# Performance work log

Hardware: AMD Instinct MI355X
Metric: run time of the kernel (lower is better)

## Reference

```python
import jax, jax.numpy as jnp
import numpy as np

B = 16      # number of point clouds
N = 16384   # points per cloud
K = 4096    # nb_vertices sampled per cloud (ratio = 0.25)


def _fps_single(pts, k):
    """Deterministic farthest-point sampling on one cloud.
    pts: [N, 3]. Start from index 0 (deterministic start), then iteratively
    pick the point with max min-distance to the selected set.
    Returns int32 indices [k].
    """
    mind0 = jnp.sum((pts - pts[0]) ** 2, axis=-1)  # [N] squared dists to seed

    def step(mind, _):
        idx = jnp.argmax(mind)                                   # farthest point
        d = jnp.sum((pts - pts[idx]) ** 2, axis=-1)              # [N]
        return jnp.minimum(mind, d), idx.astype(jnp.int32)

    _, idxs = jax.lax.scan(step, mind0, None, length=k - 1)
    return jnp.concatenate([jnp.zeros((1,), jnp.int32), idxs])


def setup_inputs() -> dict:
    key = jax.random.key(0)
    x = jax.random.normal(key, (B * N, 3), dtype=jnp.float32)
    batch = jnp.repeat(jnp.arange(B, dtype=jnp.int32), N)  # sorted cloud ids
    return {"x": x, "batch": batch}


def reference(x, batch):
    # ratio = K / N != 1, so the module runs fps and gathers.
    pts = x.reshape(B, N, 3)
    idxs = jax.vmap(lambda p: _fps_single(p, K))(pts)                 # [B, K]
    sampled = jnp.take_along_axis(pts, idxs[:, :, None], axis=1)      # [B, K, 3]
    x_out = sampled.reshape(B * K, 3)
    batch_out = jnp.repeat(jnp.arange(B, dtype=batch.dtype), K)       # [B*K]
    return (x_out, batch_out)
```

## Files before the change

kernel.cpp:

```cpp
#include <hip/hip_runtime.h>
#include <cstdint>

#pragma clang fp contract(off)

#define B_ 16
#define N_ 16384
#define K_ 4096
#define THREADS_ 1024
#define PTS_ (N_ / THREADS_)
#define NW_ (THREADS_ / 64)

#define PTS_LIST(X) \
  X(0) X(1) X(2) X(3) X(4) X(5) X(6) X(7) \
  X(8) X(9) X(10) X(11) X(12) X(13) X(14) X(15)

__device__ __forceinline__ float bfr(float f) {
  union { float f; uint32_t i; } c; c.f = f;
  c.i = (c.i + 0x7FFFu + ((c.i >> 16) & 1u)) & 0xFFFF0000u;
  return c.f;
}

template <int CTRL>
__device__ __forceinline__ unsigned long long kmax_dpp(unsigned long long k) {
  const int lo = (int)(unsigned)k;
  const int hi = (int)(unsigned)(k >> 32);
  const int plo = __builtin_amdgcn_update_dpp(lo, lo, CTRL, 0xF, 0xF, true);
  const int phi = __builtin_amdgcn_update_dpp(hi, hi, CTRL, 0xF, 0xF, true);
  const unsigned long long ok =
      ((unsigned long long)(unsigned)phi << 32) | (unsigned)plo;
  return ok > k ? ok : k;
}

__device__ __forceinline__ unsigned long long kmax_shfl(unsigned long long k, int m) {
  const int lo = __shfl_xor((int)(unsigned)k, m, 64);
  const int hi = __shfl_xor((int)(unsigned)(k >> 32), m, 64);
  const unsigned long long ok =
      ((unsigned long long)(unsigned)hi << 32) | (unsigned)lo;
  return ok > k ? ok : k;
}

__device__ __forceinline__ unsigned long long wave_kmax(unsigned long long k) {
  k = kmax_dpp<0xB1>(k);
  k = kmax_dpp<0x4E>(k);
  k = kmax_dpp<0x141>(k);
  k = kmax_dpp<0x140>(k);
  k = kmax_shfl(k, 16);
  k = kmax_shfl(k, 32);
  return k;
}

__global__ __attribute__((amdgpu_flat_work_group_size(THREADS_, THREADS_),
                          amdgpu_waves_per_eu(4, 4)))
void fps_kernel(const float* __restrict__ x, float* __restrict__ out)
{
#pragma clang fp contract(off)
  const int b    = blockIdx.x;
  const int t    = threadIdx.x;
  const int lane = t & 63;
  const int wave = t >> 6;

  __shared__ unsigned long long s_key[2][NW_];

  const float* xb  = x + (size_t)b * (N_ * 3);
  float* out_x     = out;
  float* out_batch = out + (size_t)B_ * K_ * 3;

  {
    const float bb = (float)b;
    for (int i = t; i < K_; i += THREADS_) out_batch[b * K_ + i] = bb;
  }

#define DECLP(i) float px##i, py##i, pz##i, m##i;
  PTS_LIST(DECLP)
#undef DECLP

#define LOADP(i) { const float* p_ = xb + 3 * ((i) * THREADS_ + t); \
                   px##i = p_[0]; py##i = p_[1]; pz##i = p_[2];     \
                   m##i = __builtin_inff(); }
  PTS_LIST(LOADP)
#undef LOADP

#define PINP(i) asm volatile("" : "+v"(px##i), "+v"(py##i), "+v"(pz##i), "+v"(m##i));

#define UPD(i) { const float dx_ = px##i - cx;                                  \
                 const float dy_ = py##i - cy;                                  \
                 const float dz_ = pz##i - cz;                                  \
                 const float d_  = __builtin_fmaf(dz_, dz_,                     \
                                   __builtin_fmaf(dx_, dx_, dy_ * dy_));        \
                 m##i = fminf(m##i, d_); }

#define MAXTREE(M_) { const float t0_ = fmaxf(fmaxf(m0,  m1),  m2);  \
                      const float t1_ = fmaxf(fmaxf(m3,  m4),  m5);  \
                      const float t2_ = fmaxf(fmaxf(m6,  m7),  m8);  \
                      const float t3_ = fmaxf(fmaxf(m9,  m10), m11); \
                      const float t4_ = fmaxf(fmaxf(m12, m13), m14); \
                      const float u0_ = fmaxf(fmaxf(t0_, t1_), t2_); \
                      const float u1_ = fmaxf(fmaxf(t3_, t4_), m15); \
                      M_ = fmaxf(u0_, u1_); }

#define IDXCHAIN(M_, BS_) { BS_ = 15;                                \
      if (m14 == M_) BS_ = 14; if (m13 == M_) BS_ = 13;              \
      if (m12 == M_) BS_ = 12; if (m11 == M_) BS_ = 11;              \
      if (m10 == M_) BS_ = 10; if (m9  == M_) BS_ = 9;               \
      if (m8  == M_) BS_ = 8;  if (m7  == M_) BS_ = 7;               \
      if (m6  == M_) BS_ = 6;  if (m5  == M_) BS_ = 5;               \
      if (m4  == M_) BS_ = 4;  if (m3  == M_) BS_ = 3;               \
      if (m2  == M_) BS_ = 2;  if (m1  == M_) BS_ = 1;               \
      if (m0  == M_) BS_ = 0; }

  float cx = xb[0], cy = xb[1], cz = xb[2];
  if (t == 0) {
    const uint64_t o = ((uint64_t)b * K_) * 3;
    out_x[o + 0] = bfr(cx); out_x[o + 1] = bfr(cy); out_x[o + 2] = bfr(cz);
  }

  {
    PTS_LIST(UPD)
    float bv; int bs;
    MAXTREE(bv)
    IDXCHAIN(bv, bs)
    const int bg = bs * THREADS_ + t;
    union { float f; unsigned u; } cv; cv.f = bv;
    unsigned long long key =
        ((unsigned long long)cv.u << 32) | (unsigned)~(unsigned)bg;
    key = wave_kmax(key);
    if (lane == 0) s_key[0][wave] = key;
  }
  __syncthreads();

  for (int j = 1; j < K_; ++j) {
    const int rp = (j - 1) & 1;
    const int wp = j & 1;

    PTS_LIST(PINP)

    unsigned long long k = s_key[rp][lane & 15];
    k = kmax_dpp<0xB1>(k);
    k = kmax_dpp<0x4E>(k);
    k = kmax_dpp<0x141>(k);
    k = kmax_dpp<0x140>(k);
    const unsigned idx = ~(unsigned)k;
    const int gu = __builtin_amdgcn_readfirstlane((int)idx);

    cx = xb[3 * gu + 0];
    cy = xb[3 * gu + 1];
    cz = xb[3 * gu + 2];
    if (t == 0) {
      const uint64_t o = ((uint64_t)b * K_ + j) * 3;
      out_x[o + 0] = bfr(cx); out_x[o + 1] = bfr(cy); out_x[o + 2] = bfr(cz);
    }

    PTS_LIST(UPD)
    {
      float bv; int bs;
      MAXTREE(bv)
      IDXCHAIN(bv, bs)
      const int bg = bs * THREADS_ + t;
      union { float f; unsigned u; } cv; cv.f = bv;
      unsigned long long key =
          ((unsigned long long)cv.u << 32) | (unsigned)~(unsigned)bg;
      key = wave_kmax(key);
      if (lane == 0) s_key[wp][wave] = key;
    }
    __syncthreads();
  }
#undef UPD
#undef PINP
#undef MAXTREE
#undef IDXCHAIN

}

extern "C" void kernel_launch(void* const* d_in, const int* in_sizes, int n_in,
                              void* d_out, int out_size, void* d_ws, size_t ws_size,
                              hipStream_t stream) {
  const float* x = (const float*)d_in[0];
  float* out     = (float*)d_out;
  (void)in_sizes; (void)n_in; (void)out_size; (void)d_ws; (void)ws_size;
  hipLaunchKernelGGL(fps_kernel, dim3(B_), dim3(THREADS_), 0, stream, x, out);
}
```

Before: 5.758 ms.

## Move point x/y into LDS and use two-pass DPP wave argmax

New measurement: 5.470 ms, median of 2. 5.0% less time.

```diff
diff --git a/kernel.cpp b/kernel.cpp
--- a/kernel.cpp
+++ b/kernel.cpp
@@ -21,6 +21,43 @@
 }
 
 template <int CTRL>
+__device__ __forceinline__ float dpp_fmax(float v) {
+  union { float f; int i; } s, p;
+  s.f = v;
+  p.i = __builtin_amdgcn_update_dpp(0, s.i, CTRL, 0xF, 0xF, false);
+  return fmaxf(v, p.f);
+}
+template <int CTRL>
+__device__ __forceinline__ unsigned dpp_umin(unsigned v) {
+  const int p = __builtin_amdgcn_update_dpp((int)0xFFFFFFFFu, (int)v,
+                                            CTRL, 0xF, 0xF, false);
+  const unsigned pu = (unsigned)p;
+  return pu < v ? pu : v;
+}
+
+__device__ __forceinline__ void wave_argmax(float bv, unsigned bg,
+                                            float& wv, unsigned& wg) {
+  float v = bv;
+  v = dpp_fmax<0x111>(v);
+  v = dpp_fmax<0x112>(v);
+  v = dpp_fmax<0x114>(v);
+  v = dpp_fmax<0x118>(v);
+  v = dpp_fmax<0x142>(v);
+  v = dpp_fmax<0x143>(v);
+  union { float f; int i; } mx;
+  mx.i = __builtin_amdgcn_readlane(__builtin_bit_cast(int, v), 63);
+  unsigned c = (bv == mx.f) ? bg : 0xFFFFFFFFu;
+  c = dpp_umin<0x111>(c);
+  c = dpp_umin<0x112>(c);
+  c = dpp_umin<0x114>(c);
+  c = dpp_umin<0x118>(c);
+  c = dpp_umin<0x142>(c);
+  c = dpp_umin<0x143>(c);
+  wg = (unsigned)__builtin_amdgcn_readlane((int)c, 63);
+  wv = mx.f;
+}
+
+template <int CTRL>
 __device__ __forceinline__ unsigned long long kmax_dpp(unsigned long long k) {
   const int lo = (int)(unsigned)k;
   const int hi = (int)(unsigned)(k >> 32);
@@ -29,24 +66,6 @@
   const unsigned long long ok =
       ((unsigned long long)(unsigned)phi << 32) | (unsigned)plo;
   return ok > k ? ok : k;
-}
-
-__device__ __forceinline__ unsigned long long kmax_shfl(unsigned long long k, int m) {
-  const int lo = __shfl_xor((int)(unsigned)k, m, 64);
-  const int hi = __shfl_xor((int)(unsigned)(k >> 32), m, 64);
-  const unsigned long long ok =
-      ((unsigned long long)(unsigned)hi << 32) | (unsigned)lo;
-  return ok > k ? ok : k;
-}
-
-__device__ __forceinline__ unsigned long long wave_kmax(unsigned long long k) {
-  k = kmax_dpp<0xB1>(k);
-  k = kmax_dpp<0x4E>(k);
-  k = kmax_dpp<0x141>(k);
-  k = kmax_dpp<0x140>(k);
-  k = kmax_shfl(k, 16);
-  k = kmax_shfl(k, 32);
-  return k;
 }
 
 __global__ __attribute__((amdgpu_flat_work_group_size(THREADS_, THREADS_),
@@ -59,6 +78,7 @@
   const int lane = t & 63;
   const int wave = t >> 6;
 
+  __shared__ float2 s_xy[N_];
   __shared__ unsigned long long s_key[2][NW_];
 
   const float* xb  = x + (size_t)b * (N_ * 3);
@@ -70,20 +90,20 @@
     for (int i = t; i < K_; i += THREADS_) out_batch[b * K_ + i] = bb;
   }
 
-#define DECLP(i) float px##i, py##i, pz##i, m##i;
+#define DECLP(i) float pz##i, m##i;
   PTS_LIST(DECLP)
 #undef DECLP
 
 #define LOADP(i) { const float* p_ = xb + 3 * ((i) * THREADS_ + t); \
-                   px##i = p_[0]; py##i = p_[1]; pz##i = p_[2];     \
-                   m##i = __builtin_inff(); }
+                   float2 v_; v_.x = p_[0]; v_.y = p_[1];           \
+                   s_xy[(i) * THREADS_ + t] = v_;                   \
+                   pz##i = p_[2]; m##i = __builtin_inff(); }
   PTS_LIST(LOADP)
 #undef LOADP
 
-#define PINP(i) asm volatile("" : "+v"(px##i), "+v"(py##i), "+v"(pz##i), "+v"(m##i));
-
-#define UPD(i) { const float dx_ = px##i - cx;                                  \
-                 const float dy_ = py##i - cy;                                  \
+#define UPD(i) { const float2 v_ = s_xy[(i) * THREADS_ + t];                    \
+                 const float dx_ = v_.x - cx;                                   \
+                 const float dy_ = v_.y - cy;                                   \
                  const float dz_ = pz##i - cz;                                  \
                  const float d_  = __builtin_fmaf(dz_, dz_,                     \
                                    __builtin_fmaf(dx_, dx_, dy_ * dy_));        \
@@ -108,31 +128,32 @@
       if (m2  == M_) BS_ = 2;  if (m1  == M_) BS_ = 1;               \
       if (m0  == M_) BS_ = 0; }
 
+#define REDUCE_AND_POST(PARITY) {                                        \
+      float bv; int bs;                                                  \
+      MAXTREE(bv)                                                        \
+      IDXCHAIN(bv, bs)                                                   \
+      const unsigned bg = (unsigned)(bs * THREADS_ + t);                 \
+      float wv; unsigned wg;                                             \
+      wave_argmax(bv, bg, wv, wg);                                       \
+      if (lane == 0) {                                                   \
+        union { float f; unsigned u; } cv; cv.f = wv;                    \
+        s_key[PARITY][wave] =                                            \
+            ((unsigned long long)cv.u << 32) | (unsigned)~wg;            \
+      } }
+
   float cx = xb[0], cy = xb[1], cz = xb[2];
   if (t == 0) {
     const uint64_t o = ((uint64_t)b * K_) * 3;
     out_x[o + 0] = bfr(cx); out_x[o + 1] = bfr(cy); out_x[o + 2] = bfr(cz);
   }
 
-  {
-    PTS_LIST(UPD)
-    float bv; int bs;
-    MAXTREE(bv)
-    IDXCHAIN(bv, bs)
-    const int bg = bs * THREADS_ + t;
-    union { float f; unsigned u; } cv; cv.f = bv;
-    unsigned long long key =
-        ((unsigned long long)cv.u << 32) | (unsigned)~(unsigned)bg;
-    key = wave_kmax(key);
-    if (lane == 0) s_key[0][wave] = key;
-  }
+  PTS_LIST(UPD)
+  REDUCE_AND_POST(0)
   __syncthreads();
 
   for (int j = 1; j < K_; ++j) {
     const int rp = (j - 1) & 1;
     const int wp = j & 1;
-
-    PTS_LIST(PINP)
 
     unsigned long long k = s_key[rp][lane & 15];
     k = kmax_dpp<0xB1>(k);
@@ -142,8 +163,8 @@
     const unsigned idx = ~(unsigned)k;
     const int gu = __builtin_amdgcn_readfirstlane((int)idx);
 
-    cx = xb[3 * gu + 0];
-    cy = xb[3 * gu + 1];
+    const float2 cxy = s_xy[gu];
+    cx = cxy.x; cy = cxy.y;
     cz = xb[3 * gu + 2];
     if (t == 0) {
       const uint64_t o = ((uint64_t)b * K_ + j) * 3;
@@ -151,23 +172,13 @@
     }
 
     PTS_LIST(UPD)
-    {
-      float bv; int bs;
-      MAXTREE(bv)
-      IDXCHAIN(bv, bs)
-      const int bg = bs * THREADS_ + t;
-      union { float f; unsigned u; } cv; cv.f = bv;
-      unsigned long long key =
-          ((unsigned long long)cv.u << 32) | (unsigned)~(unsigned)bg;
-      key = wave_kmax(key);
-      if (lane == 0) s_key[wp][wave] = key;
-    }
+    REDUCE_AND_POST(wp)
     __syncthreads();
   }
 #undef UPD
-#undef PINP
 #undef MAXTREE
 #undef IDXCHAIN
+#undef REDUCE_AND_POST
 
 }
 
```
